# Kernel tuning notes

Hardware: AMD Instinct MI355X
Metric: run time of the kernel (lower is better)

## Reference

```python
import jax, jax.numpy as jnp
import numpy as np

B, K, H, W, N = 256, 16, 64, 64, 1024   # batch, channels (n_ch), grid H/W, sampled sites
F_IN = 9 * K - 1                         # 3x3 neighborhood * K channels, minus center channel


def setup_inputs() -> dict:
    key = jax.random.key(0)
    ks = jax.random.split(key, 8)
    z_int = jax.random.randint(ks[0], (B, K, H, W), 0, 16, dtype=jnp.int32)
    bs = jax.random.randint(ks[1], (N,), 0, K, dtype=jnp.int32)
    ii = jax.random.randint(ks[2], (N,), 0, H, dtype=jnp.int32)
    jj = jax.random.randint(ks[3], (N,), 0, W, dtype=jnp.int32)
    W1 = jax.random.normal(ks[4], (F_IN, 128), dtype=jnp.float32) * 0.05
    b1 = jnp.zeros((128,), dtype=jnp.float32)
    W2 = jax.random.normal(ks[5], (128, 16), dtype=jnp.float32) * 0.05
    b2 = jnp.zeros((16,), dtype=jnp.float32)
    return {"z_int": z_int, "bs": bs, "ii": ii, "jj": jj,
            "W1": W1, "b1": b1, "W2": W2, "b2": b2}


def _gather_ctx(z_f, bs, ii, jj):
    # Faithful to get_context ordering: loops di, dj (each in [-1,0,1]) then b,
    # skipping (di==0, dj==0, b==bi). Flattened skip position = 4*K + bi.
    off = jnp.array([-1, 0, 1], dtype=jnp.int32)
    di = jnp.repeat(off, 3)          # [9]
    dj = jnp.tile(off, 3)            # [9]
    ni = (ii[:, None] + di[None, :]) % H   # [N, 9] toroidal wrap
    nj = (jj[:, None] + dj[None, :]) % W   # [N, 9]
    ctx = z_f[:, :, ni, nj]                # [B, K, N, 9]
    ctx = jnp.transpose(ctx, (2, 0, 3, 1)).reshape(N, B, 9 * K)  # [N, B, 9K], (di,dj) major then b
    drop = 4 * K + bs                      # [N] center-channel flat index
    idx = jnp.arange(F_IN, dtype=jnp.int32)
    keep = idx[None, :] + (idx[None, :] >= drop[:, None]).astype(jnp.int32)  # [N, F_IN]
    return jax.vmap(lambda c, k: c[:, k])(ctx, keep)  # [N, B, F_IN]


def reference(z_int, bs, ii, jj, W1, b1, W2, b2):
    z_f = z_int.astype(jnp.float32) / 15.0
    ctx = _gather_ctx(z_f, bs, ii, jj)                 # [N, B, 9K-1]
    h = jax.nn.relu(jnp.einsum('nbf,fh->nbh', ctx, W1) + b1)
    logits = jnp.einsum('nbh,hc->nbc', h, W2) + b2     # [N, B, 16]
    pred = jnp.argmax(logits, axis=-1)                 # [N, B]
    tgt = z_int[:, bs, ii, jj].T                       # [N, B]
    rate = jnp.mean((pred != tgt).astype(jnp.float32)) # np.mean of per-site mean == global mean
    return rate
```

## Files before the change

kernel.cpp:

```cpp
#include <hip/hip_runtime.h>
#include <stdint.h>

#define NB 1024
#define BB 256
#define KK 16
#define HH 64
#define WW 64
#define F_FULL 144
#define HDIM 128
#define CDIM 16
#define KPAD 160
#define APITCH 168
#define HPITCH 136

typedef __bf16 bf16x8 __attribute__((ext_vector_type(8)));
typedef float f32x4 __attribute__((ext_vector_type(4)));

#define W1T_OFF 256
#define W1T_BYTES (16 * HDIM * KPAD * 2)
#define W2B_OFF (W1T_OFF + W1T_BYTES)
#define W2B_BYTES (CDIM * HDIM * 2)
#define ZT_OFF (W2B_OFF + W2B_BYTES)

__device__ __forceinline__ unsigned short bf16_bits(float v) {
    __bf16 b = (__bf16)v;
    return __builtin_bit_cast(unsigned short, b);
}

#define TP 144
__global__ __launch_bounds__(256) void prep_kernel(
    const int* __restrict__ z, const float* __restrict__ W1,
    const float* __restrict__ W2, uint8_t* __restrict__ zt,
    unsigned short* __restrict__ W1t, unsigned short* __restrict__ W2b,
    int* __restrict__ counters) {
    int bid = blockIdx.x;
    int t = threadIdx.x;
    if (bid < 4096) {
        __shared__ uint8_t tile[32 * TP];
        int bx = bid & 127;
        int by = bid >> 7;
        int c0 = bx * 32, r0 = by * 128;
#pragma unroll
        for (int i = 0; i < 4; ++i) {
            int lin = i * 256 + t;
            int c = lin & 31;
            int rq = lin >> 5;
            uchar4 v;
            v.x = (uint8_t)z[(size_t)(r0 + rq * 4 + 0) * 4096 + c0 + c];
            v.y = (uint8_t)z[(size_t)(r0 + rq * 4 + 1) * 4096 + c0 + c];
            v.z = (uint8_t)z[(size_t)(r0 + rq * 4 + 2) * 4096 + c0 + c];
            v.w = (uint8_t)z[(size_t)(r0 + rq * 4 + 3) * 4096 + c0 + c];
            *(uchar4*)(tile + c * TP + rq * 4) = v;
        }
        __syncthreads();
        int cy = t >> 3, rx = t & 7;
        uint4 v = *(const uint4*)(tile + cy * TP + rx * 16);
        *(uint4*)(zt + (size_t)(c0 + cy) * 4096 + r0 + rx * 16) = v;
    } else if (bid < 5376) {
        int idx = (bid - 4096) * 256 + t;
        int k = idx % KPAD;
        int h = (idx / KPAD) % HDIM;
        int s = idx / (KPAD * HDIM);
        int drop = 4 * KK + s;
        float val = 0.0f;
        if (k < F_FULL && k != drop) {
            int src = k - (k > drop ? 1 : 0);
            val = W1[src * HDIM + h];
        }
        W1t[idx] = bf16_bits(val);
    } else {
        int idx = (bid - 5376) * 256 + t;
        if (idx < CDIM * HDIM) {
            int k = idx % HDIM;
            int c = idx / HDIM;
            W2b[idx] = bf16_bits(W2[k * CDIM + c]);
        }
        if (bid == 5376 && t == 0) counters[0] = 0;
    }
}

__global__ __launch_bounds__(256, 3) void main_kernel(
    const uint8_t* __restrict__ zt, const unsigned short* __restrict__ W1t,
    const float* __restrict__ b1, const unsigned short* __restrict__ W2b,
    const float* __restrict__ b2, const int* __restrict__ bs,
    const int* __restrict__ ii, const int* __restrict__ jj,
    int* __restrict__ counters) {
    __shared__ __align__(16) unsigned char smem[21760];
    unsigned short* sA = (unsigned short*)smem;
    unsigned short* sH = (unsigned short*)smem;
    float* slg = (float*)(smem + 64 * HPITCH * 2);

    int t = threadIdx.x;
    int bid = blockIdx.x;
    int n = bid >> 2;
    int b_base = (bid & 3) << 6;
    int wave = t >> 6, lane = t & 63;
    int l15 = lane & 15, l4 = lane >> 4;

    int in_ = ii[n], jn = jj[n], sn = bs[n];

    if (t < 192) {
        int b = t / 3, part = t % 3;
        *(uint4*)(sA + b * APITCH + F_FULL + part * 8) = make_uint4(0, 0, 0, 0);
    }

    const unsigned short* w1s = W1t + (size_t)sn * (HDIM * KPAD);
    int n0 = wave * 32;
    bf16x8 Bf[2][5];
#pragma unroll
    for (int nt = 0; nt < 2; ++nt)
#pragma unroll
        for (int ks = 0; ks < 5; ++ks)
            Bf[nt][ks] = *(const bf16x8*)(w1s + (n0 + nt * 16 + l15) * KPAD + ks * 32 + l4 * 8);
    bf16x8 Bf2[4];
#pragma unroll
    for (int ks = 0; ks < 4; ++ks)
        Bf2[ks] = *(const bf16x8*)(W2b + l15 * HDIM + ks * 32 + l4 * 8);
    float b1v0 = b1[n0 + l15], b1v1 = b1[n0 + 16 + l15];
    float b2v = b2[l15];

    for (int item = t; item < 9 * 64; item += 256) {
        int p = item >> 6;
        int b = item & 63;
        int di = p / 3 - 1, dj = p % 3 - 1;
        int ni = (in_ + di + HH) & (HH - 1);
        int nj = (jn + dj + WW) & (WW - 1);
        const uint8_t* src = zt + (((size_t)(ni * WW + nj) * BB + (b_base + b)) << 4);
        uint4 raw = *(const uint4*)src;
        const uint8_t* bytes = (const uint8_t*)&raw;
        union { __bf16 h[16]; uint4 q[2]; } u;
#pragma unroll
        for (int k = 0; k < 16; ++k)
            u.h[k] = (__bf16)((float)bytes[k] * (1.0f / 15.0f));
        uint4* dst = (uint4*)(sA + b * APITCH + p * 16);
        dst[0] = u.q[0];
        dst[1] = u.q[1];
    }
    __syncthreads();

    f32x4 acc[4][2] = {};
#pragma unroll
    for (int mt = 0; mt < 4; ++mt) {
        bf16x8 Af[5];
#pragma unroll
        for (int ks = 0; ks < 5; ++ks)
            Af[ks] = *(const bf16x8*)(sA + (mt * 16 + l15) * APITCH + ks * 32 + l4 * 8);
#pragma unroll
        for (int ks = 0; ks < 5; ++ks) {
            acc[mt][0] = __builtin_amdgcn_mfma_f32_16x16x32_bf16(Af[ks], Bf[0][ks], acc[mt][0], 0, 0, 0);
            acc[mt][1] = __builtin_amdgcn_mfma_f32_16x16x32_bf16(Af[ks], Bf[1][ks], acc[mt][1], 0, 0, 0);
        }
    }
    __syncthreads();

#pragma unroll
    for (int mt = 0; mt < 4; ++mt)
#pragma unroll
        for (int nt = 0; nt < 2; ++nt) {
            float bv = nt ? b1v1 : b1v0;
            int hcol = n0 + nt * 16 + l15;
#pragma unroll
            for (int r = 0; r < 4; ++r) {
                int b = mt * 16 + l4 * 4 + r;
                float v = fmaxf(acc[mt][nt][r] + bv, 0.0f);
                sH[b * HPITCH + hcol] = bf16_bits(v);
            }
        }
    __syncthreads();

    f32x4 acc2 = {};
#pragma unroll
    for (int ks = 0; ks < 4; ++ks) {
        bf16x8 Af = *(const bf16x8*)(sH + (wave * 16 + l15) * HPITCH + ks * 32 + l4 * 8);
        acc2 = __builtin_amdgcn_mfma_f32_16x16x32_bf16(Af, Bf2[ks], acc2, 0, 0, 0);
    }
#pragma unroll
    for (int r = 0; r < 4; ++r) {
        int b = wave * 16 + l4 * 4 + r;
        slg[b * 17 + l15] = acc2[r] + b2v;
    }
    __syncthreads();

    if (t < 64) {
        float best = slg[t * 17];
        int pi = 0;
#pragma unroll
        for (int c = 1; c < CDIM; ++c) {
            float v = slg[t * 17 + c];
            if (v > best) { best = v; pi = c; }
        }
        int tgt = zt[(((size_t)(in_ * WW + jn) * BB + b_base + t) << 4) + sn];
        unsigned long long m = __ballot(pi != tgt);
        if (t == 0) atomicAdd(&counters[0], (int)__popcll(m));
    }
}

__global__ void finalize_kernel(const int* __restrict__ counters, float* __restrict__ out) {
    out[0] = (float)(counters[0]) / (float)(NB * BB);
}

extern "C" void kernel_launch(void* const* d_in, const int* in_sizes, int n_in,
                              void* d_out, int out_size, void* d_ws, size_t ws_size,
                              hipStream_t stream) {
    const int* z = (const int*)d_in[0];
    const int* bs = (const int*)d_in[1];
    const int* ii = (const int*)d_in[2];
    const int* jj = (const int*)d_in[3];
    const float* W1 = (const float*)d_in[4];
    const float* b1 = (const float*)d_in[5];
    const float* W2 = (const float*)d_in[6];
    const float* b2 = (const float*)d_in[7];
    float* out = (float*)d_out;

    uint8_t* ws = (uint8_t*)d_ws;
    int* counters = (int*)ws;
    unsigned short* W1t = (unsigned short*)(ws + W1T_OFF);
    unsigned short* W2b = (unsigned short*)(ws + W2B_OFF);
    uint8_t* zt = ws + ZT_OFF;

    prep_kernel<<<5384, 256, 0, stream>>>(z, W1, W2, zt, W1t, W2b, counters);
    main_kernel<<<NB * 4, 256, 0, stream>>>(zt, W1t, b1, W2b, b2, bs, ii, jj, counters);
    finalize_kernel<<<1, 1, 0, stream>>>(counters, out);
}
```

Measured before the change: 162.4 us.

## Loop each block over four batch tiles with double-buffered gather prefetch

Each main-kernel block now handles one site across all 256 batch entries in four 64-row tiles, instead of one tile per block. The next tile's neighborhood bytes are loaded into registers during compute and written to an alternate LDS buffer. This amortizes the per-block W1/W2 fragment loads and index reads, and reduces global atomics to one per site. In exchange, LDS per block roughly doubles and there are 4x fewer blocks, which may reduce occupancy and latency hiding.

```diff
diff --git a/kernel.cpp b/kernel.cpp
--- a/kernel.cpp
+++ b/kernel.cpp
@@ -12,6 +12,7 @@
 #define KPAD 160
 #define APITCH 168
 #define HPITCH 136
+#define ABYTES (64 * APITCH * 2)
 
 typedef __bf16 bf16x8 __attribute__((ext_vector_type(8)));
 typedef float f32x4 __attribute__((ext_vector_type(4)));
@@ -85,24 +86,17 @@
     const float* __restrict__ b2, const int* __restrict__ bs,
     const int* __restrict__ ii, const int* __restrict__ jj,
     int* __restrict__ counters) {
-    __shared__ __align__(16) unsigned char smem[21760];
-    unsigned short* sA = (unsigned short*)smem;
-    unsigned short* sH = (unsigned short*)smem;
-    float* slg = (float*)(smem + 64 * HPITCH * 2);
+    __shared__ __align__(16) unsigned char smem[2 * ABYTES + 64 * 17 * 4];
+    unsigned short* sA0 = (unsigned short*)smem;
+    unsigned short* sA1 = (unsigned short*)(smem + ABYTES);
+    float* slg = (float*)(smem + 2 * ABYTES);
 
     int t = threadIdx.x;
-    int bid = blockIdx.x;
-    int n = bid >> 2;
-    int b_base = (bid & 3) << 6;
+    int n = blockIdx.x;
     int wave = t >> 6, lane = t & 63;
     int l15 = lane & 15, l4 = lane >> 4;
 
     int in_ = ii[n], jn = jj[n], sn = bs[n];
-
-    if (t < 192) {
-        int b = t / 3, part = t % 3;
-        *(uint4*)(sA + b * APITCH + F_FULL + part * 8) = make_uint4(0, 0, 0, 0);
-    }
 
     const unsigned short* w1s = W1t + (size_t)sn * (HDIM * KPAD);
     int n0 = wave * 32;
@@ -119,80 +113,119 @@
     float b1v0 = b1[n0 + l15], b1v1 = b1[n0 + 16 + l15];
     float b2v = b2[l15];
 
-    for (int item = t; item < 9 * 64; item += 256) {
-        int p = item >> 6;
-        int b = item & 63;
-        int di = p / 3 - 1, dj = p % 3 - 1;
-        int ni = (in_ + di + HH) & (HH - 1);
-        int nj = (jn + dj + WW) & (WW - 1);
-        const uint8_t* src = zt + (((size_t)(ni * WW + nj) * BB + (b_base + b)) << 4);
-        uint4 raw = *(const uint4*)src;
-        const uint8_t* bytes = (const uint8_t*)&raw;
-        union { __bf16 h[16]; uint4 q[2]; } u;
-#pragma unroll
-        for (int k = 0; k < 16; ++k)
-            u.h[k] = (__bf16)((float)bytes[k] * (1.0f / 15.0f));
-        uint4* dst = (uint4*)(sA + b * APITCH + p * 16);
-        dst[0] = u.q[0];
-        dst[1] = u.q[1];
+    if (t < 192) {
+        int b = t / 3, part = t % 3;
+        *(uint4*)(sA0 + b * APITCH + F_FULL + part * 8) = make_uint4(0, 0, 0, 0);
+        *(uint4*)(sA1 + b * APITCH + F_FULL + part * 8) = make_uint4(0, 0, 0, 0);
     }
-    __syncthreads();
-
-    f32x4 acc[4][2] = {};
-#pragma unroll
-    for (int mt = 0; mt < 4; ++mt) {
-        bf16x8 Af[5];
-#pragma unroll
-        for (int ks = 0; ks < 5; ++ks)
-            Af[ks] = *(const bf16x8*)(sA + (mt * 16 + l15) * APITCH + ks * 32 + l4 * 8);
-#pragma unroll
-        for (int ks = 0; ks < 5; ++ks) {
-            acc[mt][0] = __builtin_amdgcn_mfma_f32_16x16x32_bf16(Af[ks], Bf[0][ks], acc[mt][0], 0, 0, 0);
-            acc[mt][1] = __builtin_amdgcn_mfma_f32_16x16x32_bf16(Af[ks], Bf[1][ks], acc[mt][1], 0, 0, 0);
-        }
+
+    uint4 g0, g1, g2;
+    auto gload = [&](int tile) {
+        int b = (t & 63) + tile * 64;
+        int p0 = t >> 6;
+        int ni0 = (in_ + p0 / 3 - 1) & (HH - 1);
+        int nj0 = (jn + p0 % 3 - 1) & (WW - 1);
+        g0 = *(const uint4*)(zt + (((size_t)(ni0 * WW + nj0) * BB + b) << 4));
+        int p1 = p0 + 4;
+        int ni1 = (in_ + p1 / 3 - 1) & (HH - 1);
+        int nj1 = (jn + p1 % 3 - 1) & (WW - 1);
+        g1 = *(const uint4*)(zt + (((size_t)(ni1 * WW + nj1) * BB + b) << 4));
+        if (t < 64) {
+            int ni2 = (in_ + 1) & (HH - 1);
+            int nj2 = (jn + 1) & (WW - 1);
+            g2 = *(const uint4*)(zt + (((size_t)(ni2 * WW + nj2) * BB + b) << 4));
+        }
+    };
+    auto gwrite = [&](unsigned short* dst) {
+        int b = t & 63;
+        int p0 = t >> 6;
+        auto conv = [&](uint4 raw, int p) {
+            const uint8_t* bytes = (const uint8_t*)&raw;
+            union { __bf16 h[16]; uint4 q[2]; } u;
+#pragma unroll
+            for (int k = 0; k < 16; ++k)
+                u.h[k] = (__bf16)((float)bytes[k] * (1.0f / 15.0f));
+            uint4* d = (uint4*)(dst + b * APITCH + p * 16);
+            d[0] = u.q[0];
+            d[1] = u.q[1];
+        };
+        conv(g0, p0);
+        conv(g1, p0 + 4);
+        if (t < 64) conv(g2, 8);
+    };
+
+    gload(0);
+    gwrite(sA0);
+    int local_err = 0;
+
+    for (int tile = 0; tile < 4; ++tile) {
+        unsigned short* sA = (tile & 1) ? sA1 : sA0;
+        unsigned short* sH = sA;
+        unsigned short* sAnext = (tile & 1) ? sA0 : sA1;
+
+        if (tile < 3) gload(tile + 1);
+        __syncthreads();
+
+        f32x4 acc[4][2] = {};
+#pragma unroll
+        for (int mt = 0; mt < 4; ++mt) {
+            bf16x8 Af[5];
+#pragma unroll
+            for (int ks = 0; ks < 5; ++ks)
+                Af[ks] = *(const bf16x8*)(sA + (mt * 16 + l15) * APITCH + ks * 32 + l4 * 8);
+#pragma unroll
+            for (int ks = 0; ks < 5; ++ks) {
+                acc[mt][0] = __builtin_amdgcn_mfma_f32_16x16x32_bf16(Af[ks], Bf[0][ks], acc[mt][0], 0, 0, 0);
+                acc[mt][1] = __builtin_amdgcn_mfma_f32_16x16x32_bf16(Af[ks], Bf[1][ks], acc[mt][1], 0, 0, 0);
+            }
+        }
+        __syncthreads();
+
+#pragma unroll
+        for (int mt = 0; mt < 4; ++mt)
+#pragma unroll
+            for (int nt = 0; nt < 2; ++nt) {
+                float bv = nt ? b1v1 : b1v0;
+                int hcol = n0 + nt * 16 + l15;
+#pragma unroll
+                for (int r = 0; r < 4; ++r) {
+                    int b = mt * 16 + l4 * 4 + r;
+                    float v = fmaxf(acc[mt][nt][r] + bv, 0.0f);
+                    sH[b * HPITCH + hcol] = bf16_bits(v);
+                }
+            }
+        __syncthreads();
+
+        f32x4 acc2 = {};
+#pragma unroll
+        for (int ks = 0; ks < 4; ++ks) {
+            bf16x8 Af = *(const bf16x8*)(sH + (wave * 16 + l15) * HPITCH + ks * 32 + l4 * 8);
+            acc2 = __builtin_amdgcn_mfma_f32_16x16x32_bf16(Af, Bf2[ks], acc2, 0, 0, 0);
+        }
+#pragma unroll
+        for (int r = 0; r < 4; ++r) {
+            int b = wave * 16 + l4 * 4 + r;
+            slg[b * 17 + l15] = acc2[r] + b2v;
+        }
+        __syncthreads();
+
+        if (t < 64) {
+            float best = slg[t * 17];
+            int pi = 0;
+#pragma unroll
+            for (int c = 1; c < CDIM; ++c) {
+                float v = slg[t * 17 + c];
+                if (v > best) { best = v; pi = c; }
+            }
+            int bglob = tile * 64 + t;
+            int tgt = zt[(((size_t)(in_ * WW + jn) * BB + bglob) << 4) + sn];
+            unsigned long long m = __ballot(pi != tgt);
+            if (t == 0) local_err += (int)__popcll(m);
+        }
+        if (tile < 3) gwrite(sAnext);
     }
-    __syncthreads();
-
-#pragma unroll
-    for (int mt = 0; mt < 4; ++mt)
-#pragma unroll
-        for (int nt = 0; nt < 2; ++nt) {
-            float bv = nt ? b1v1 : b1v0;
-            int hcol = n0 + nt * 16 + l15;
-#pragma unroll
-            for (int r = 0; r < 4; ++r) {
-                int b = mt * 16 + l4 * 4 + r;
-                float v = fmaxf(acc[mt][nt][r] + bv, 0.0f);
-                sH[b * HPITCH + hcol] = bf16_bits(v);
-            }
-        }
-    __syncthreads();
-
-    f32x4 acc2 = {};
-#pragma unroll
-    for (int ks = 0; ks < 4; ++ks) {
-        bf16x8 Af = *(const bf16x8*)(sH + (wave * 16 + l15) * HPITCH + ks * 32 + l4 * 8);
-        acc2 = __builtin_amdgcn_mfma_f32_16x16x32_bf16(Af, Bf2[ks], acc2, 0, 0, 0);
-    }
-#pragma unroll
-    for (int r = 0; r < 4; ++r) {
-        int b = wave * 16 + l4 * 4 + r;
-        slg[b * 17 + l15] = acc2[r] + b2v;
-    }
-    __syncthreads();
-
-    if (t < 64) {
-        float best = slg[t * 17];
-        int pi = 0;
-#pragma unroll
-        for (int c = 1; c < CDIM; ++c) {
-            float v = slg[t * 17 + c];
-            if (v > best) { best = v; pi = c; }
-        }
-        int tgt = zt[(((size_t)(in_ * WW + jn) * BB + b_base + t) << 4) + sn];
-        unsigned long long m = __ballot(pi != tgt);
-        if (t == 0) atomicAdd(&counters[0], (int)__popcll(m));
-    }
+
+    if (t == 0) atomicAdd(&counters[0], local_err);
 }
 
 __global__ void finalize_kernel(const int* __restrict__ counters, float* __restrict__ out) {
@@ -219,6 +252,6 @@
     uint8_t* zt = ws + ZT_OFF;
 
     prep_kernel<<<5384, 256, 0, stream>>>(z, W1, W2, zt, W1t, W2b, counters);
-    main_kernel<<<NB * 4, 256, 0, stream>>>(zt, W1t, b1, W2b, b2, bs, ii, jj, counters);
+    main_kernel<<<NB, 256, 0, stream>>>(zt, W1t, b1, W2b, b2, bs, ii, jj, counters);
     finalize_kernel<<<1, 1, 0, stream>>>(counters, out);
 }
```

After: 132.7 us, median of 2. -18.3%, faster.
